# Performance work log

Measured on AMD Instinct MI355X. Metric: run time of the kernel, lower is better.

## Reference

```python
import jax, jax.numpy as jnp
import numpy as np

B, D, T, DA, H = 64, 1500, 1000, 512, 1

def setup_inputs() -> dict:
    key = jax.random.key(0)
    k1, k2, k3 = jax.random.split(key, 3)
    # xavier_uniform bounds
    lim1 = float(np.sqrt(6.0 / (D + DA)))
    lim2 = float(np.sqrt(6.0 / (DA + H)))
    return {
        "input_feature": jax.random.normal(k1, (B, D, T), dtype=jnp.float32),
        "w_1": jax.random.uniform(k2, (D, DA), dtype=jnp.float32, minval=-lim1, maxval=lim1),
        "bias_1": jnp.zeros((DA,), dtype=jnp.float32),
        "w_2": jax.random.uniform(k3, (DA, H), dtype=jnp.float32, minval=-lim2, maxval=lim2),
        "bias_2": jnp.zeros((H,), dtype=jnp.float32),
    }

def reference(input_feature, w_1, bias_1, w_2, bias_2):
    # input_feature: [B, D, T]
    x_t = jnp.swapaxes(input_feature, 1, 2)              # [B, T, D]
    hidden = jax.nn.relu(jnp.einsum('btd,da->bta', x_t, w_1) + bias_1)  # [B, T, DA]
    scores = jnp.einsum('bta,ah->bth', hidden, w_2) + bias_2            # [B, T, H]
    A = jax.nn.softmax(scores, axis=1)                                  # softmax over time
    E = jnp.einsum('bdt,bth->bdh', input_feature, A)                    # weighted mean [B, D, H]
    sq = jnp.einsum('bdt,bth->bdh', input_feature * input_feature, A)   # weighted E[x^2]
    std = jnp.sqrt(jax.nn.relu(sq - E * E) + 1e-05)                     # [B, D, H]
    layer_out = jnp.concatenate((E, std), axis=1).reshape(input_feature.shape[0], -1)  # [B, 2*D*H]
    return (A, layer_out)
```

## Files before the change

### kernel.cpp

```cpp
#include <hip/hip_runtime.h>
#include <hip/hip_bf16.h>

#define NB 64
#define ND 1500
#define NT 1000
#define NA 512
#define KSTEPS 47
#define STR 17

typedef __bf16 bf16x8 __attribute__((ext_vector_type(8)));
typedef float  f32x4  __attribute__((ext_vector_type(4)));

union BQ { unsigned u[4]; bf16x8 v; };

static __device__ __forceinline__ unsigned pack2(float lo, float hi) {
    __bf16 l = (__bf16)lo, h = (__bf16)hi;
    unsigned short lu = __builtin_bit_cast(unsigned short, l);
    unsigned short hu = __builtin_bit_cast(unsigned short, h);
    return ((unsigned)hu << 16) | (unsigned)lu;
}

__global__ void w1p_kernel(const float* __restrict__ w1, __bf16* __restrict__ w1p) {
    int g = blockIdx.x * 256 + threadIdx.x;
    if (g >= KSTEPS * 32 * 64) return;
    int lane = g & 63;
    int a16  = (g >> 6) & 31;
    int ks   = g >> 11;
    int col = lane & 15, quad = lane >> 4;
    int a  = a16 * 16 + col;
    int d0 = ks * 32 + quad * 8;
    bf16x8 o;
    #pragma unroll
    for (int j = 0; j < 8; ++j) {
        int d = d0 + j;
        o[j] = (d < ND) ? (__bf16)w1[d * NA + a] : (__bf16)0.0f;
    }
    *(bf16x8*)(w1p + (size_t)g * 8) = o;
}

__global__ __launch_bounds__(256, 2) void score_kernel(
    const float* __restrict__ X,
    const __bf16* __restrict__ w1p,
    const float* __restrict__ b1,
    const float* __restrict__ w2,
    float* __restrict__ scores)
{
    __shared__ unsigned Bs[2][64 * STR];
    __shared__ float b1s[NA], w2s[NA];
    __shared__ float ssc[64];

    const int tt = blockIdx.x;
    const int b  = blockIdx.y;
    const int t0 = tt * 64;
    const int tid = threadIdx.x;

    for (int i = tid; i < NA; i += 256) { b1s[i] = b1[i]; w2s[i] = w2[i]; }

    const int lane = tid & 63;
    const int wave = tid >> 6;
    const int col = lane & 15;
    const int quad = lane >> 4;

    const int dr2  = tid >> 4;
    const int toff = (tid & 15) << 2;
    const float* xbase = X + (size_t)b * (ND * NT) + (t0 + toff);
    const bool tval = (t0 + toff) < NT;

    const __bf16* wlane = w1p + (size_t)(wave * 8) * 512 + (size_t)lane * 8;

    f32x4 acc[8][4];
    #pragma unroll
    for (int u = 0; u < 8; ++u)
        #pragma unroll
        for (int i = 0; i < 4; ++i)
            acc[u][i] = (f32x4){0.f, 0.f, 0.f, 0.f};

    {
        float4 g0 = {0,0,0,0}, g1 = {0,0,0,0};
        int d0 = 2 * dr2, d1 = d0 + 1;
        if (tval && d0 < ND) g0 = *(const float4*)(xbase + (size_t)d0 * NT);
        if (tval && d1 < ND) g1 = *(const float4*)(xbase + (size_t)d1 * NT);
        Bs[0][(toff + 0) * STR + dr2] = pack2(g0.x, g1.x);
        Bs[0][(toff + 1) * STR + dr2] = pack2(g0.y, g1.y);
        Bs[0][(toff + 2) * STR + dr2] = pack2(g0.z, g1.z);
        Bs[0][(toff + 3) * STR + dr2] = pack2(g0.w, g1.w);
    }
    float4 c0 = {0,0,0,0}, c1 = {0,0,0,0};
    {
        int d0 = 32 + 2 * dr2, d1 = d0 + 1;
        if (tval && d0 < ND) c0 = *(const float4*)(xbase + (size_t)d0 * NT);
        if (tval && d1 < ND) c1 = *(const float4*)(xbase + (size_t)d1 * NT);
    }

    for (int ks = 0; ks < KSTEPS; ++ks) {
        const int cur = ks & 1;

        bf16x8 af[8];
        const __bf16* wk = wlane + (size_t)ks * (32 * 64 * 8);
        #pragma unroll
        for (int u = 0; u < 8; ++u)
            af[u] = *(const bf16x8*)(wk + (size_t)u * 512);

        float4 n0 = {0,0,0,0}, n1 = {0,0,0,0};
        {
            int d0 = ks * 32 + 64 + 2 * dr2, d1 = d0 + 1;
            if (tval && d0 < ND) n0 = *(const float4*)(xbase + (size_t)d0 * NT);
            if (tval && d1 < ND) n1 = *(const float4*)(xbase + (size_t)d1 * NT);
        }

        asm volatile("s_waitcnt lgkmcnt(0)" ::: "memory");
        __builtin_amdgcn_s_barrier();

        bf16x8 bq[4];
        #pragma unroll
        for (int i = 0; i < 4; ++i) {
            int tl = i * 16 + col;
            BQ q;
            #pragma unroll
            for (int jp = 0; jp < 4; ++jp)
                q.u[jp] = Bs[cur][tl * STR + quad * 4 + jp];
            bq[i] = q.v;
        }

        #pragma unroll
        for (int u = 0; u < 8; ++u)
            #pragma unroll
            for (int i = 0; i < 4; ++i)
                acc[u][i] = __builtin_amdgcn_mfma_f32_16x16x32_bf16(af[u], bq[i], acc[u][i], 0, 0, 0);

        Bs[cur ^ 1][(toff + 0) * STR + dr2] = pack2(c0.x, c1.x);
        Bs[cur ^ 1][(toff + 1) * STR + dr2] = pack2(c0.y, c1.y);
        Bs[cur ^ 1][(toff + 2) * STR + dr2] = pack2(c0.z, c1.z);
        Bs[cur ^ 1][(toff + 3) * STR + dr2] = pack2(c0.w, c1.w);

        c0 = n0; c1 = n1;
    }

    float part[4] = {0.f, 0.f, 0.f, 0.f};
    #pragma unroll
    for (int u = 0; u < 8; ++u)
        #pragma unroll
        for (int r = 0; r < 4; ++r) {
            int a = wave * 128 + u * 16 + quad * 4 + r;
            float bb = b1s[a], ww = w2s[a];
            #pragma unroll
            for (int i = 0; i < 4; ++i) {
                float h = acc[u][i][r] + bb;
                part[i] += fmaxf(h, 0.f) * ww;
            }
        }

    __syncthreads();
    if (tid < 64) ssc[tid] = 0.f;
    __syncthreads();
    #pragma unroll
    for (int i = 0; i < 4; ++i) {
        float p = part[i];
        p += __shfl_down(p, 32);
        p += __shfl_down(p, 16);
        if (quad == 0) atomicAdd(&ssc[i * 16 + col], p);
    }
    __syncthreads();
    if (tid < 64) {
        int t = t0 + tid;
        if (t < NT) scores[b * NT + t] = ssc[tid];
    }
}

__global__ __launch_bounds__(256) void softmax_kernel(
    const float* __restrict__ scores, float* __restrict__ A_out)
{
    __shared__ float red[256];
    const int b = blockIdx.x, tid = threadIdx.x;
    const float* s = scores + b * NT;
    float v[4], m = -1e30f;
    #pragma unroll
    for (int i = 0; i < 4; ++i) {
        int t = tid + i * 256;
        v[i] = (t < NT) ? s[t] : -1e30f;
        m = fmaxf(m, v[i]);
    }
    red[tid] = m; __syncthreads();
    for (int off = 128; off > 0; off >>= 1) {
        if (tid < off) red[tid] = fmaxf(red[tid], red[tid + off]);
        __syncthreads();
    }
    m = red[0]; __syncthreads();
    float sum = 0.f;
    #pragma unroll
    for (int i = 0; i < 4; ++i) {
        v[i] = __expf(v[i] - m);
        if (tid + i * 256 < NT) sum += v[i]; else v[i] = 0.f;
    }
    red[tid] = sum; __syncthreads();
    for (int off = 128; off > 0; off >>= 1) {
        if (tid < off) red[tid] += red[tid + off];
        __syncthreads();
    }
    float inv = 1.f / red[0];
    #pragma unroll
    for (int i = 0; i < 4; ++i) {
        int t = tid + i * 256;
        if (t < NT) A_out[b * NT + t] = v[i] * inv;
    }
}

__global__ __launch_bounds__(256) void pool_kernel(
    const float* __restrict__ X, const float* __restrict__ A,
    float* __restrict__ outE)
{
    __shared__ float As[NT];
    const int b = blockIdx.x;
    const int d0 = blockIdx.y << 2;
    const int tid = threadIdx.x;
    for (int t = tid; t < NT; t += 256) As[t] = A[b * NT + t];
    __syncthreads();
    const int wave = tid >> 6, lane = tid & 63;
    const int d = d0 + wave;
    const float* x = X + (size_t)b * (ND * NT) + (size_t)d * NT;
    float e = 0.f, q = 0.f;
    #pragma unroll
    for (int it = 0; it < 4; ++it) {
        int t = it * 256 + (lane << 2);
        if (t < NT) {
            float4 xv = *(const float4*)(x + t);
            float4 a4 = *(const float4*)(As + t);
            e += xv.x * a4.x + xv.y * a4.y + xv.z * a4.z + xv.w * a4.w;
            q += xv.x * xv.x * a4.x + xv.y * xv.y * a4.y + xv.z * xv.z * a4.z + xv.w * xv.w * a4.w;
        }
    }
    #pragma unroll
    for (int off = 32; off > 0; off >>= 1) {
        e += __shfl_down(e, off);
        q += __shfl_down(q, off);
    }
    if (lane == 0) {
        outE[b * 3000 + d] = e;
        outE[b * 3000 + 1500 + d] = sqrtf(fmaxf(q - e * e, 0.f) + 1e-5f);
    }
}

extern "C" void kernel_launch(void* const* d_in, const int* in_sizes, int n_in,
                              void* d_out, int out_size, void* d_ws, size_t ws_size,
                              hipStream_t stream) {
    const float* X  = (const float*)d_in[0];
    const float* w1 = (const float*)d_in[1];
    const float* b1 = (const float*)d_in[2];
    const float* w2 = (const float*)d_in[3];

    char* ws = (char*)d_ws;
    __bf16* w1p    = (__bf16*)ws;
    float*  scores = (float*)(ws + (size_t)KSTEPS * 32 * 64 * 8 * 2);

    float* out = (float*)d_out;

    w1p_kernel<<<(KSTEPS * 32 * 64 + 255) / 256, 256, 0, stream>>>(w1, w1p);
    score_kernel<<<dim3(16, NB), 256, 0, stream>>>(X, w1p, b1, w2, scores);
    softmax_kernel<<<NB, 256, 0, stream>>>(scores, out);
    pool_kernel<<<dim3(NB, ND / 4), 256, 0, stream>>>(X, out, out + NB * NT);
}
```

Baseline: 629.1 us.

## Widen score tile to 128 timesteps and stage pool rows through LDS

The score kernel now uses 512-thread blocks covering 128 timesteps, with each wave owning 64 hidden units. This halves how often each w1 fragment is re-read from global memory per timestep and replaces the shared-memory atomic reduction with a per-wave buffer summed at the end. The pool kernel now has each block handle 64 feature rows, staging 64-timestep chunks of X through LDS, and each thread accumulates partial sums for one row instead of doing a full wave shuffle reduction per row. The cost is fewer score blocks (512 in total) with more waves each, extra barriers per chunk in the pool kernel, and some wasted padding work on the last row block.

```diff
diff --git a/kernel.cpp b/kernel.cpp
--- a/kernel.cpp
+++ b/kernel.cpp
@@ -7,6 +7,8 @@
 #define NA 512
 #define KSTEPS 47
 #define STR 17
+#define TT 128
+#define NTT 8
 
 typedef __bf16 bf16x8 __attribute__((ext_vector_type(8)));
 typedef float  f32x4  __attribute__((ext_vector_type(4)));
@@ -38,41 +40,41 @@
     *(bf16x8*)(w1p + (size_t)g * 8) = o;
 }
 
-__global__ __launch_bounds__(256, 2) void score_kernel(
+__global__ __launch_bounds__(512, 2) void score_kernel(
     const float* __restrict__ X,
     const __bf16* __restrict__ w1p,
     const float* __restrict__ b1,
     const float* __restrict__ w2,
     float* __restrict__ scores)
 {
-    __shared__ unsigned Bs[2][64 * STR];
+    __shared__ unsigned Bs[2][TT * STR];
     __shared__ float b1s[NA], w2s[NA];
-    __shared__ float ssc[64];
+    __shared__ float wred[8][TT];
 
     const int tt = blockIdx.x;
     const int b  = blockIdx.y;
-    const int t0 = tt * 64;
+    const int t0 = tt * TT;
     const int tid = threadIdx.x;
 
-    for (int i = tid; i < NA; i += 256) { b1s[i] = b1[i]; w2s[i] = w2[i]; }
+    for (int i = tid; i < NA; i += 512) { b1s[i] = b1[i]; w2s[i] = w2[i]; }
 
     const int lane = tid & 63;
     const int wave = tid >> 6;
     const int col = lane & 15;
     const int quad = lane >> 4;
 
-    const int dr2  = tid >> 4;
-    const int toff = (tid & 15) << 2;
+    const int dr2  = tid >> 5;
+    const int toff = (tid & 31) << 2;
     const float* xbase = X + (size_t)b * (ND * NT) + (t0 + toff);
     const bool tval = (t0 + toff) < NT;
 
-    const __bf16* wlane = w1p + (size_t)(wave * 8) * 512 + (size_t)lane * 8;
-
-    f32x4 acc[8][4];
-    #pragma unroll
-    for (int u = 0; u < 8; ++u)
-        #pragma unroll
-        for (int i = 0; i < 4; ++i)
+    const __bf16* wlane = w1p + (size_t)(wave * 4) * 512 + (size_t)lane * 8;
+
+    f32x4 acc[4][8];
+    #pragma unroll
+    for (int u = 0; u < 4; ++u)
+        #pragma unroll
+        for (int i = 0; i < 8; ++i)
             acc[u][i] = (f32x4){0.f, 0.f, 0.f, 0.f};
 
     {
@@ -95,10 +97,10 @@
     for (int ks = 0; ks < KSTEPS; ++ks) {
         const int cur = ks & 1;
 
-        bf16x8 af[8];
+        bf16x8 af[4];
         const __bf16* wk = wlane + (size_t)ks * (32 * 64 * 8);
         #pragma unroll
-        for (int u = 0; u < 8; ++u)
+        for (int u = 0; u < 4; ++u)
             af[u] = *(const bf16x8*)(wk + (size_t)u * 512);
 
         float4 n0 = {0,0,0,0}, n1 = {0,0,0,0};
@@ -111,9 +113,9 @@
         asm volatile("s_waitcnt lgkmcnt(0)" ::: "memory");
         __builtin_amdgcn_s_barrier();
 
-        bf16x8 bq[4];
-        #pragma unroll
-        for (int i = 0; i < 4; ++i) {
+        bf16x8 bq[8];
+        #pragma unroll
+        for (int i = 0; i < 8; ++i) {
             int tl = i * 16 + col;
             BQ q;
             #pragma unroll
@@ -123,9 +125,9 @@
         }
 
         #pragma unroll
-        for (int u = 0; u < 8; ++u)
+        for (int u = 0; u < 4; ++u)
             #pragma unroll
-            for (int i = 0; i < 4; ++i)
+            for (int i = 0; i < 8; ++i)
                 acc[u][i] = __builtin_amdgcn_mfma_f32_16x16x32_bf16(af[u], bq[i], acc[u][i], 0, 0, 0);
 
         Bs[cur ^ 1][(toff + 0) * STR + dr2] = pack2(c0.x, c1.x);
@@ -136,34 +138,34 @@
         c0 = n0; c1 = n1;
     }
 
-    float part[4] = {0.f, 0.f, 0.f, 0.f};
-    #pragma unroll
-    for (int u = 0; u < 8; ++u)
+    float part[8] = {0.f, 0.f, 0.f, 0.f, 0.f, 0.f, 0.f, 0.f};
+    #pragma unroll
+    for (int u = 0; u < 4; ++u)
         #pragma unroll
         for (int r = 0; r < 4; ++r) {
-            int a = wave * 128 + u * 16 + quad * 4 + r;
+            int a = wave * 64 + u * 16 + quad * 4 + r;
             float bb = b1s[a], ww = w2s[a];
             #pragma unroll
-            for (int i = 0; i < 4; ++i) {
+            for (int i = 0; i < 8; ++i) {
                 float h = acc[u][i][r] + bb;
                 part[i] += fmaxf(h, 0.f) * ww;
             }
         }
 
-    __syncthreads();
-    if (tid < 64) ssc[tid] = 0.f;
-    __syncthreads();
-    #pragma unroll
-    for (int i = 0; i < 4; ++i) {
+    #pragma unroll
+    for (int i = 0; i < 8; ++i) {
         float p = part[i];
         p += __shfl_down(p, 32);
         p += __shfl_down(p, 16);
-        if (quad == 0) atomicAdd(&ssc[i * 16 + col], p);
+        if (quad == 0) wred[wave][i * 16 + col] = p;
     }
     __syncthreads();
-    if (tid < 64) {
+    if (tid < TT) {
+        float s = 0.f;
+        #pragma unroll
+        for (int w = 0; w < 8; ++w) s += wred[w][tid];
         int t = t0 + tid;
-        if (t < NT) scores[b * NT + t] = ssc[tid];
+        if (t < NT) scores[b * NT + t] = s;
     }
 }
 
@@ -205,38 +207,65 @@
     }
 }
 
+#define DBLK 64
+#define TC 64
+#define NCH 16
 __global__ __launch_bounds__(256) void pool_kernel(
     const float* __restrict__ X, const float* __restrict__ A,
     float* __restrict__ outE)
 {
-    __shared__ float As[NT];
+    __shared__ float As[1024];
+    __shared__ float Xs[DBLK][68];
     const int b = blockIdx.x;
-    const int d0 = blockIdx.y << 2;
+    const int d0 = blockIdx.y * DBLK;
     const int tid = threadIdx.x;
-    for (int t = tid; t < NT; t += 256) As[t] = A[b * NT + t];
+
+    for (int t = tid; t < 1024; t += 256) As[t] = (t < NT) ? A[b * NT + t] : 0.f;
+
+    const int lrow = tid >> 2, lseg = tid & 3;
+    const int r = tid & 63, w = tid >> 6;
+    const float* xrow = X + (size_t)b * (ND * NT) + (size_t)(d0 + lrow) * NT;
+    const bool rowv = (d0 + lrow) < ND;
+
+    float e = 0.f, q = 0.f;
+    for (int ch = 0; ch < NCH; ++ch) {
+        const int tc = ch * TC;
+        float4 v[4];
+        #pragma unroll
+        for (int j = 0; j < 4; ++j) {
+            int t = tc + j * 16 + lseg * 4;
+            v[j] = (rowv && t < NT) ? *(const float4*)(xrow + t) : (float4){0.f, 0.f, 0.f, 0.f};
+        }
+        __syncthreads();
+        #pragma unroll
+        for (int j = 0; j < 4; ++j)
+            *(float4*)(&Xs[lrow][j * 16 + lseg * 4]) = v[j];
+        __syncthreads();
+        #pragma unroll
+        for (int j = 0; j < 4; ++j) {
+            float4 x4 = *(const float4*)(&Xs[r][w * 16 + j * 4]);
+            float4 a4 = *(const float4*)(&As[tc + w * 16 + j * 4]);
+            float xa;
+            xa = x4.x * a4.x; e += xa; q += x4.x * xa;
+            xa = x4.y * a4.y; e += xa; q += x4.y * xa;
+            xa = x4.z * a4.z; e += xa; q += x4.z * xa;
+            xa = x4.w * a4.w; e += xa; q += x4.w * xa;
+        }
+    }
+
     __syncthreads();
-    const int wave = tid >> 6, lane = tid & 63;
-    const int d = d0 + wave;
-    const float* x = X + (size_t)b * (ND * NT) + (size_t)d * NT;
-    float e = 0.f, q = 0.f;
-    #pragma unroll
-    for (int it = 0; it < 4; ++it) {
-        int t = it * 256 + (lane << 2);
-        if (t < NT) {
-            float4 xv = *(const float4*)(x + t);
-            float4 a4 = *(const float4*)(As + t);
-            e += xv.x * a4.x + xv.y * a4.y + xv.z * a4.z + xv.w * a4.w;
-            q += xv.x * xv.x * a4.x + xv.y * xv.y * a4.y + xv.z * xv.z * a4.z + xv.w * xv.w * a4.w;
-        }
-    }
-    #pragma unroll
-    for (int off = 32; off > 0; off >>= 1) {
-        e += __shfl_down(e, off);
-        q += __shfl_down(q, off);
-    }
-    if (lane == 0) {
-        outE[b * 3000 + d] = e;
-        outE[b * 3000 + 1500 + d] = sqrtf(fmaxf(q - e * e, 0.f) + 1e-5f);
+    float* red = &Xs[0][0];
+    red[w * 64 + r] = e;
+    red[256 + w * 64 + r] = q;
+    __syncthreads();
+    if (tid < DBLK) {
+        float ee = red[tid] + red[64 + tid] + red[128 + tid] + red[192 + tid];
+        float qq = red[256 + tid] + red[320 + tid] + red[384 + tid] + red[448 + tid];
+        int d = d0 + tid;
+        if (d < ND) {
+            outE[b * 3000 + d] = ee;
+            outE[b * 3000 + 1500 + d] = sqrtf(fmaxf(qq - ee * ee, 0.f) + 1e-5f);
+        }
     }
 }
 
@@ -255,7 +284,7 @@
     float* out = (float*)d_out;
 
     w1p_kernel<<<(KSTEPS * 32 * 64 + 255) / 256, 256, 0, stream>>>(w1, w1p);
-    score_kernel<<<dim3(16, NB), 256, 0, stream>>>(X, w1p, b1, w2, scores);
+    score_kernel<<<dim3(NTT, NB), 512, 0, stream>>>(X, w1p, b1, w2, scores);
     softmax_kernel<<<NB, 256, 0, stream>>>(scores, out);
-    pool_kernel<<<dim3(NB, ND / 4), 256, 0, stream>>>(X, out, out + NB * NT);
-}
+    pool_kernel<<<dim3(NB, (ND + DBLK - 1) / DBLK), 256, 0, stream>>>(X, out, out + NB * NT);
+}
```

Result: no change. 635.6 us (+1.0%).
